# Performance work log

Measured on AMD Instinct MI355X. Metric: run time of the kernel, lower is better.

The kernel has to match this reference:

```python
import jax, jax.numpy as jnp
import numpy as np

B, H, W, C = 4, 256, 256, 32
K = 5  # per-pixel kernel spatial size (K*K = 25 taps)


def setup_inputs() -> dict:
    key = jax.random.key(0)
    k1, k2, k3 = jax.random.split(key, 3)
    feat = jax.random.normal(k1, (B, H, W, C), dtype=jnp.float32)
    kernel = jax.random.normal(k2, (B, H, W, K * K), dtype=jnp.float32)
    bias = jax.random.normal(k3, (C,), dtype=jnp.float32)
    return {"feat": feat, "kernel": kernel, "bias": bias}


def reference(feat, kernel, bias):
    # Per-pixel predicted convolution (kernel prediction network style):
    # out[b,h,w,c] = sum_{i,j} feat[b, h+i-p, w+j-p, c] * kernel[b,h,w, i*K+j]
    # Kernel taps are shared across channels; SAME zero padding.
    b, h, w, c = feat.shape
    kk = kernel.shape[-1]
    k = int(round(np.sqrt(kk)))
    pad = k // 2
    fp = jnp.pad(feat, ((0, 0), (pad, pad), (pad, pad), (0, 0)))
    out = jnp.zeros_like(feat)
    for i in range(k):          # small fixed K*K loop; avoids materializing
        for j in range(k):      # the [B,H,W,K*K,C] patch tensor
            tap = kernel[..., i * k + j][..., None]          # [B,H,W,1]
            out = out + fp[:, i:i + h, j:j + w, :] * tap      # [B,H,W,C]
    return out + bias  # tf.nn.bias_add, channels_last
```

## Files before the change

### kernel.cpp

```cpp
#include <hip/hip_runtime.h>


#define BB 4
#define HH 256
#define WW 256
#define CC 32
#define KK 5
#define PADR 2
#define PPB 32
#define TPB 256

__global__ __launch_bounds__(TPB) void kpn_conv_kernel(
    const float* __restrict__ feat,
    const float* __restrict__ kern,
    const float* __restrict__ bias,
    float* __restrict__ out)
{
    __shared__ float sk[PPB * KK * KK];

    const int t  = threadIdx.x;
    const int p0 = blockIdx.x * PPB;

    const float* kbase = kern + (size_t)p0 * (KK * KK);
    for (int idx = t; idx < PPB * KK * KK; idx += TPB) {
        sk[idx] = kbase[idx];
    }
    __syncthreads();

    const int pixLocal = t >> 3;
    const int cg       = (t & 7) * 4;
    const int p  = p0 + pixLocal;
    const int b  = p >> 16;
    const int hw = p & 65535;
    const int h  = hw >> 8;
    const int w  = hw & 255;

    float4 acc = *(const float4*)(bias + cg);

    const float* fb  = feat + (((size_t)b) << 16) * CC;
    const float* skp = sk + pixLocal * (KK * KK);

    #pragma unroll
    for (int i = 0; i < KK; ++i) {
        const int hh = h + i - PADR;
        const bool hv = (unsigned)hh < (unsigned)HH;
        #pragma unroll
        for (int j = 0; j < KK; ++j) {
            const int ww = w + j - PADR;
            const float wgt = skp[i * KK + j];
            if (hv && (unsigned)ww < (unsigned)WW) {
                const float4 f =
                    *(const float4*)(fb + ((((size_t)hh << 8) + ww) << 5) + cg);
                acc.x += f.x * wgt;
                acc.y += f.y * wgt;
                acc.z += f.z * wgt;
                acc.w += f.w * wgt;
            }
        }
    }

    *(float4*)(out + (((size_t)p) << 5) + cg) = acc;
}

extern "C" void kernel_launch(void* const* d_in, const int* in_sizes, int n_in,
                              void* d_out, int out_size, void* d_ws, size_t ws_size,
                              hipStream_t stream) {
    const float* feat = (const float*)d_in[0];
    const float* kern = (const float*)d_in[1];
    const float* bias = (const float*)d_in[2];
    float* out = (float*)d_out;

    const int nPix = BB * HH * WW;
    dim3 grid(nPix / PPB);
    dim3 block(TPB);
    kpn_conv_kernel<<<grid, block, 0, stream>>>(feat, kern, bias, out);
}
```

Baseline: 125.2 us.

## Tile blocks as 4x32 pixel patches and reuse feature rows across vertical outputs

Each block now covers a 4-row by 32-column pixel tile, and each thread accumulates four vertically stacked outputs. Every loaded feature row of five float4 taps feeds all output rows that need it, so per-thread feature loads drop from 25 per output to 40 per four outputs. Kernel taps are staged into shared memory with float4 loads. The cost is more registers for four accumulators and five feature vectors, which may lower occupancy, and the grid has fewer blocks.

```diff
diff --git a/kernel.cpp b/kernel.cpp
--- a/kernel.cpp
+++ b/kernel.cpp
@@ -6,8 +6,8 @@
 #define WW 256
 #define CC 32
 #define KK 5
-#define PADR 2
-#define PPB 32
+#define VH 4
+#define TW 32
 #define TPB 256
 
 __global__ __launch_bounds__(TPB) void kpn_conv_kernel(
@@ -16,50 +16,81 @@
     const float* __restrict__ bias,
     float* __restrict__ out)
 {
-    __shared__ float sk[PPB * KK * KK];
+    __shared__ float sk[VH * TW * KK * KK];
 
-    const int t  = threadIdx.x;
-    const int p0 = blockIdx.x * PPB;
+    const int t = threadIdx.x;
 
-    const float* kbase = kern + (size_t)p0 * (KK * KK);
-    for (int idx = t; idx < PPB * KK * KK; idx += TPB) {
-        sk[idx] = kbase[idx];
+    const int bw = blockIdx.x & 7;
+    const int bh = (blockIdx.x >> 3) & 63;
+    const int b  = blockIdx.x >> 9;
+    const int h0 = bh * VH;
+    const int w0 = bw * TW;
+
+    const float* kb = kern + ((size_t)((b * HH + h0) * WW + w0)) * (KK * KK);
+    #pragma unroll
+    for (int it = 0; it < 4; ++it) {
+        int idx = t + it * TPB;
+        if (idx < VH * TW * KK * KK / 4) {
+            int row = idx / 200;
+            int off = (idx - row * 200) * 4;
+            *(float4*)(sk + row * (TW * KK * KK) + off) =
+                *(const float4*)(kb + (size_t)row * WW * KK * KK + off);
+        }
     }
     __syncthreads();
 
-    const int pixLocal = t >> 3;
-    const int cg       = (t & 7) * 4;
-    const int p  = p0 + pixLocal;
-    const int b  = p >> 16;
-    const int hw = p & 65535;
-    const int h  = hw >> 8;
-    const int w  = hw & 255;
+    const int cg = (t & 7) * 4;
+    const int wL = t >> 3;
+    const int w  = w0 + wL;
 
-    float4 acc = *(const float4*)(bias + cg);
+    const float4 bz = *(const float4*)(bias + cg);
+    float4 acc[VH];
+    #pragma unroll
+    for (int oh = 0; oh < VH; ++oh) acc[oh] = bz;
 
-    const float* fb  = feat + (((size_t)b) << 16) * CC;
-    const float* skp = sk + pixLocal * (KK * KK);
+    const float* fb = feat + (((size_t)b) << 16) * CC;
 
     #pragma unroll
-    for (int i = 0; i < KK; ++i) {
-        const int hh = h + i - PADR;
-        const bool hv = (unsigned)hh < (unsigned)HH;
-        #pragma unroll
-        for (int j = 0; j < KK; ++j) {
-            const int ww = w + j - PADR;
-            const float wgt = skp[i * KK + j];
-            if (hv && (unsigned)ww < (unsigned)WW) {
-                const float4 f =
-                    *(const float4*)(fb + ((((size_t)hh << 8) + ww) << 5) + cg);
-                acc.x += f.x * wgt;
-                acc.y += f.y * wgt;
-                acc.z += f.z * wgt;
-                acc.w += f.w * wgt;
+    for (int r = 0; r < VH + KK - 1; ++r) {
+        const int hh = h0 + r - (KK / 2);
+        if ((unsigned)hh < (unsigned)HH) {
+            float4 f[KK];
+            #pragma unroll
+            for (int j = 0; j < KK; ++j) {
+                int ww  = w + j - (KK / 2);
+                int wwc = min(max(ww, 0), WW - 1);
+                f[j] = *(const float4*)(fb + ((((size_t)hh << 8) + wwc) << 5) + cg);
+            }
+            #pragma unroll
+            for (int j = 0; j < KK; ++j) {
+                int ww = w + j - (KK / 2);
+                if ((unsigned)ww >= (unsigned)WW) {
+                    f[j].x = 0.f; f[j].y = 0.f; f[j].z = 0.f; f[j].w = 0.f;
+                }
+            }
+            #pragma unroll
+            for (int oh = 0; oh < VH; ++oh) {
+                const int ii = r - oh;
+                if (ii >= 0 && ii < KK) {
+                    const float* wp = sk + oh * (TW * KK * KK) + wL * (KK * KK) + ii * KK;
+                    #pragma unroll
+                    for (int j = 0; j < KK; ++j) {
+                        const float wg = wp[j];
+                        acc[oh].x += f[j].x * wg;
+                        acc[oh].y += f[j].y * wg;
+                        acc[oh].z += f[j].z * wg;
+                        acc[oh].w += f[j].w * wg;
+                    }
+                }
             }
         }
     }
 
-    *(float4*)(out + (((size_t)p) << 5) + cg) = acc;
+    #pragma unroll
+    for (int oh = 0; oh < VH; ++oh) {
+        const size_t pix = (size_t)(b * HH + h0 + oh) * WW + w;
+        *(float4*)(out + pix * CC + cg) = acc[oh];
+    }
 }
 
 extern "C" void kernel_launch(void* const* d_in, const int* in_sizes, int n_in,
@@ -70,8 +101,7 @@
     const float* bias = (const float*)d_in[2];
     float* out = (float*)d_out;
 
-    const int nPix = BB * HH * WW;
-    dim3 grid(nPix / PPB);
+    dim3 grid(BB * (HH / VH) * (WW / TW));
     dim3 block(TPB);
     kpn_conv_kernel<<<grid, block, 0, stream>>>(feat, kern, bias, out);
 }
```

After: 117.2 us. -6.4%, faster.
